# Performance work log

Hardware: AMD Instinct MI355X
Metric: run time of the kernel (lower is better)

Reference implementation:

```python
import jax, jax.numpy as jnp
import numpy as np

HIDDEN = 512

def setup_inputs() -> dict:
    key = jax.random.key(0)
    ks = jax.random.split(key, 8)
    B, T, H = 64, 2048, HIDDEN
    s_ih = 1.0 / np.sqrt(H)
    inp = {
        'x': jax.random.normal(ks[0], (B, T, 1), dtype=jnp.float32),
        # PyTorch LSTM params, gate order (i, f, g, o)
        'W_ih': jax.random.uniform(ks[1], (4 * H, 1), jnp.float32, -s_ih, s_ih),
        'W_hh': jax.random.uniform(ks[2], (4 * H, H), jnp.float32, -s_ih, s_ih),
        'b_ih': jax.random.uniform(ks[3], (4 * H,), jnp.float32, -s_ih, s_ih),
        'b_hh': jax.random.uniform(ks[4], (4 * H,), jnp.float32, -s_ih, s_ih),
        'W_fc': jax.random.uniform(ks[5], (1, H), jnp.float32, -s_ih, s_ih),
        'b_fc': jax.random.uniform(ks[6], (1,), jnp.float32, -s_ih, s_ih),
    }
    return inp


def _lstm(x, W_ih, W_hh, b_ih, b_hh):
    # x: [B, T, 1] -> scan over time
    B, T, _ = x.shape
    H = W_hh.shape[1]
    # precompute input projection for all timesteps: [T, B, 4H]
    x_proj = jnp.einsum('bti,gi->tbg', x, W_ih) + (b_ih + b_hh)

    def step(carry, xp_t):
        h, c = carry
        gates = xp_t + h @ W_hh.T  # [B, 4H]
        i, f, g, o = jnp.split(gates, 4, axis=-1)
        i = jax.nn.sigmoid(i)
        f = jax.nn.sigmoid(f)
        g = jnp.tanh(g)
        o = jax.nn.sigmoid(o)
        c = f * c + i * g
        h = o * jnp.tanh(c)
        return (h, c), h

    h0 = jnp.zeros((B, H), x.dtype)
    c0 = jnp.zeros((B, H), x.dtype)
    (h_n, c_n), hs = jax.lax.scan(step, (h0, c0), x_proj)
    out = jnp.transpose(hs, (1, 0, 2))  # [B, T, H]
    return out, h_n, c_n


def reference(x, W_ih, W_hh, b_ih, b_hh, W_fc, b_fc):
    out, h_n, c_n = _lstm(x, W_ih, W_hh, b_ih, b_hh)
    y = out @ W_fc.T + b_fc  # [B, T, 1]
    # h_n/c_n shaped [num_layers, B, H] like torch
    return y, h_n[None], c_n[None]
```

## Files before the change

### kernel.cpp

```cpp
#include <hip/hip_runtime.h>


#define TT 2048
#define BB 64
#define HH 512
#define GB 8
#define NBLK 32
#define DEPTH 4
#define PLANE (GB * HH)
#define CPAD 16
#define DYN_LDS 86016
#define Y_OFF 0
#define HN_OFF (BB * TT)
#define CN_OFF (BB * TT + BB * HH)

typedef short short8 __attribute__((ext_vector_type(8)));
typedef float f32x4  __attribute__((ext_vector_type(4)));

__device__ __forceinline__ unsigned f2bf(float f) {
    unsigned u = __float_as_uint(f);
    return (u + 0x7fffu + ((u >> 16) & 1u)) >> 16;
}
__device__ __forceinline__ float bf2f(unsigned h) { return __uint_as_float(h << 16); }

__device__ __forceinline__ unsigned ld_agent(const unsigned* p) {
    return __hip_atomic_load(p, __ATOMIC_RELAXED, __HIP_MEMORY_SCOPE_AGENT);
}
__device__ __forceinline__ void st_agent(unsigned* p, unsigned v) {
    __hip_atomic_store(p, v, __ATOMIC_RELAXED, __HIP_MEMORY_SCOPE_AGENT);
}
__device__ __forceinline__ unsigned add_agent(unsigned* p, unsigned v) {
    return __hip_atomic_fetch_add(p, v, __ATOMIC_RELAXED, __HIP_MEMORY_SCOPE_AGENT);
}

__device__ __forceinline__ void ld_sc0_8x128(const void* pa, const void* pb,
                                             short8* A, short8* B) {
    asm volatile(
        "global_load_dwordx4 %0, %[pa], off sc0\n\t"
        "global_load_dwordx4 %1, %[pa], off offset:64 sc0\n\t"
        "global_load_dwordx4 %2, %[pa], off offset:128 sc0\n\t"
        "global_load_dwordx4 %3, %[pa], off offset:192 sc0\n\t"
        "global_load_dwordx4 %4, %[pb], off sc0\n\t"
        "global_load_dwordx4 %5, %[pb], off offset:64 sc0\n\t"
        "global_load_dwordx4 %6, %[pb], off offset:128 sc0\n\t"
        "global_load_dwordx4 %7, %[pb], off offset:192 sc0\n\t"
        "s_waitcnt vmcnt(0)"
        : "=&v"(A[0]), "=&v"(A[1]), "=&v"(A[2]), "=&v"(A[3]),
          "=&v"(B[0]), "=&v"(B[1]), "=&v"(B[2]), "=&v"(B[3])
        : [pa] "v"(pa), [pb] "v"(pb)
        : "memory");
}
__device__ __forceinline__ void ld_mall_8x128(const void* pa, const void* pb,
                                              short8* A, short8* B) {
    asm volatile(
        "global_load_dwordx4 %0, %[pa], off sc0 sc1\n\t"
        "global_load_dwordx4 %1, %[pa], off offset:64 sc0 sc1\n\t"
        "global_load_dwordx4 %2, %[pa], off offset:128 sc0 sc1\n\t"
        "global_load_dwordx4 %3, %[pa], off offset:192 sc0 sc1\n\t"
        "global_load_dwordx4 %4, %[pb], off sc0 sc1\n\t"
        "global_load_dwordx4 %5, %[pb], off offset:64 sc0 sc1\n\t"
        "global_load_dwordx4 %6, %[pb], off offset:128 sc0 sc1\n\t"
        "global_load_dwordx4 %7, %[pb], off offset:192 sc0 sc1\n\t"
        "s_waitcnt vmcnt(0)"
        : "=&v"(A[0]), "=&v"(A[1]), "=&v"(A[2]), "=&v"(A[3]),
          "=&v"(B[0]), "=&v"(B[1]), "=&v"(B[2]), "=&v"(B[3])
        : [pa] "v"(pa), [pb] "v"(pb)
        : "memory");
}
__device__ __forceinline__ uint4 ld_sc0_probe(const void* p) {
    uint4 d;
    asm volatile("global_load_dwordx4 %0, %1, off sc0\n\ts_waitcnt vmcnt(0)"
                 : "=&v"(d) : "v"(p) : "memory");
    return d;
}

#define GSP(w, tl, r, c) gsp[((((w) * 4 + (tl)) * 16 + (r)) * 20) + (c)]

template <bool FAST>
__device__ __noinline__ void run_loop(
    const float* __restrict__ x, const float* __restrict__ Whh,
    const float* __restrict__ Wih, const float* __restrict__ bih,
    const float* __restrict__ bhh, const float* __restrict__ Wfc,
    const float* __restrict__ bfc, float* __restrict__ out,
    unsigned short* __restrict__ hb, unsigned* __restrict__ stepc,
    const int grp, const int ut, float* gsp)
{
    const int tid  = threadIdx.x;
    const int wid  = tid >> 6;
    const int lane = tid & 63;
    const int quad = lane >> 4;
    const int l16  = lane & 15;

    short8 whi[4][4], wlo[4][4];
#pragma unroll
    for (int tl = 0; tl < 4; ++tl) {
        const int grow  = tl * HH + ut * 16 + l16;
        const float* wr = Whh + grow * HH + wid * 128 + quad * 8;
#pragma unroll
        for (int ki = 0; ki < 4; ++ki) {
            const float* wp = wr + ki * 32;
            short8 h8, l8;
#pragma unroll
            for (int j = 0; j < 8; ++j) {
                const float f = wp[j];
                const unsigned hi = f2bf(f);
                h8[j] = (short)hi;
                l8[j] = (short)f2bf(f - bf2f(hi));
            }
            whi[tl][ki] = h8;
            wlo[tl][ki] = l8;
        }
    }

    const int b2    = (tid >> 4) & 7;
    const int u     = tid & 15;
    const int bglob = grp * GB + b2;
    const int ug    = ut * 16 + u;
    float wih4[4], bia4[4];
#pragma unroll
    for (int gi = 0; gi < 4; ++gi) {
        const int grow = gi * HH + ug;
        wih4[gi] = Wih[grow];
        bia4[gi] = bih[grow] + bhh[grow];
    }
    const float wfc  = Wfc[ug];
    const float bfcv = bfc[0];
    float c = 0.0f;

    const int base_hi = grp * 2 * DEPTH;
    const int base_lo = base_hi + DEPTH;
    unsigned* hb32 = (unsigned*)hb;

    const unsigned* pollp = stepc + (unsigned)((wid * 8 + (lane & 7)) * CPAD);

    int fuse = 1 << 24;

    for (int t = 0; t < TT; ++t) {
        const float xv = x[bglob * TT + t];

        {
            const unsigned tgt = (unsigned)t;
            for (;;) {
                unsigned v = 0xFFFFFFFFu;
                if (lane < 8) v = ld_agent(pollp);
                if (__all((int)(v >= tgt))) break;
                if (--fuse <= 0) break;
            }
        }

        const unsigned short* Ah =
            hb + (base_hi + (t & 3)) * PLANE + (l16 & 7) * HH + wid * 128 + quad * 8;
        const unsigned short* Al =
            hb + (base_lo + (t & 3)) * PLANE + (l16 & 7) * HH + wid * 128 + quad * 8;
        short8 ah[4], al[4];
        if constexpr (FAST) {
            ld_sc0_8x128(Ah, Al, ah, al);
        } else {
            ld_mall_8x128(Ah, Al, ah, al);
        }

        f32x4 acc[4] = {{0.f,0.f,0.f,0.f},{0.f,0.f,0.f,0.f},
                        {0.f,0.f,0.f,0.f},{0.f,0.f,0.f,0.f}};
#pragma unroll
        for (int ki = 0; ki < 4; ++ki) {
#pragma unroll
            for (int tl = 0; tl < 4; ++tl)
                acc[tl] = __builtin_amdgcn_mfma_f32_16x16x32_bf16(ah[ki], whi[tl][ki], acc[tl], 0, 0, 0);
#pragma unroll
            for (int tl = 0; tl < 4; ++tl)
                acc[tl] = __builtin_amdgcn_mfma_f32_16x16x32_bf16(al[ki], whi[tl][ki], acc[tl], 0, 0, 0);
#pragma unroll
            for (int tl = 0; tl < 4; ++tl)
                acc[tl] = __builtin_amdgcn_mfma_f32_16x16x32_bf16(ah[ki], wlo[tl][ki], acc[tl], 0, 0, 0);
        }
#pragma unroll
        for (int tl = 0; tl < 4; ++tl)
#pragma unroll
            for (int r = 0; r < 4; ++r)
                GSP(wid, tl, quad * 4 + r, l16) = acc[tl][r];
        __syncthreads();

        if (tid < 128) {
            float pre[4];
#pragma unroll
            for (int gi = 0; gi < 4; ++gi) {
                float s = 0.f;
#pragma unroll
                for (int w = 0; w < 4; ++w) s += GSP(w, gi, b2, u);
                pre[gi] = fmaf(xv, wih4[gi], bia4[gi]) + s;
            }
            const float ig = 1.f / (1.f + __expf(-pre[0]));
            const float fg = 1.f / (1.f + __expf(-pre[1]));
            const float gg = 2.f / (1.f + __expf(-2.f * pre[2])) - 1.f;
            const float og = 1.f / (1.f + __expf(-pre[3]));
            c = fmaf(fg, c, ig * gg);
            const float tc = 2.f / (1.f + __expf(-2.f * c)) - 1.f;
            const float h  = og * tc;

            const unsigned hh = f2bf(h);
            const unsigned hl = f2bf(h - bf2f(hh));
            const unsigned packed = hh | (hl << 16);
            const unsigned part = (unsigned)__shfl_xor((int)packed, 1, 64);
            if ((u & 1) == 0) {
                const unsigned sH = __builtin_amdgcn_perm(part, packed, 0x05040100u);
                const unsigned sL = __builtin_amdgcn_perm(part, packed, 0x07060302u);
                const int slot    = (t + 1) & 3;
                const int pairidx = (b2 * HH + ug) >> 1;
                if constexpr (FAST) {
                    __hip_atomic_store(hb32 + (base_hi + slot) * (PLANE / 2) + pairidx, sH,
                                       __ATOMIC_RELAXED, __HIP_MEMORY_SCOPE_WORKGROUP);
                    __hip_atomic_store(hb32 + (base_lo + slot) * (PLANE / 2) + pairidx, sL,
                                       __ATOMIC_RELAXED, __HIP_MEMORY_SCOPE_WORKGROUP);
                } else {
                    __hip_atomic_store(hb32 + (base_hi + slot) * (PLANE / 2) + pairidx, sH,
                                       __ATOMIC_RELAXED, __HIP_MEMORY_SCOPE_AGENT);
                    __hip_atomic_store(hb32 + (base_lo + slot) * (PLANE / 2) + pairidx, sL,
                                       __ATOMIC_RELAXED, __HIP_MEMORY_SCOPE_AGENT);
                }
            }

            float yp = h * wfc;
            yp += __shfl_down(yp, 8, 16);
            yp += __shfl_down(yp, 4, 16);
            yp += __shfl_down(yp, 2, 16);
            yp += __shfl_down(yp, 1, 16);
            if (u == 0) {
                if (ut == 0) yp += bfcv;
                if constexpr (FAST)
                    __hip_atomic_fetch_add(out + Y_OFF + bglob * TT + t, yp,
                                           __ATOMIC_RELAXED, __HIP_MEMORY_SCOPE_WORKGROUP);
                else
                    atomicAdd(out + Y_OFF + bglob * TT + t, yp);
            }
            if (t == TT - 1) {
                out[HN_OFF + bglob * HH + ug] = h;
                out[CN_OFF + bglob * HH + ug] = c;
            }
        }
        __syncthreads();
        if (tid == 0) st_agent(stepc + ut * CPAD, (unsigned)(t + 1));
    }
}

__global__ __launch_bounds__(256, 1)
void lstm_xcd(const float* __restrict__ x, const float* __restrict__ Wih,
              const float* __restrict__ Whh, const float* __restrict__ bih,
              const float* __restrict__ bhh, const float* __restrict__ Wfc,
              const float* __restrict__ bfc, float* __restrict__ out,
              unsigned short* __restrict__ hb, unsigned* __restrict__ cnt)
{
    __shared__ int s_grp, s_ut, s_fast;
    extern __shared__ float gsp[];

    const int tid = threadIdx.x;
    unsigned* claim = cnt + 4096;
    unsigned* bar1  = cnt + 4136;

    if (tid == 0) {
        unsigned xcc;
        asm volatile("s_getreg_b32 %0, hwreg(HW_REG_XCC_ID)" : "=s"(xcc));
        xcc &= 7u;
        const unsigned slot = add_agent(claim + xcc, 1u);
        asm volatile("s_waitcnt vmcnt(0)" ::: "memory");
        add_agent(bar1, 1u);
        int bfuse = 1 << 22;
        while (ld_agent(bar1) < 256u) {
            __builtin_amdgcn_s_sleep(1);
            if (--bfuse <= 0) break;
        }
        bool pure = (bfuse > 0);
        for (int g2 = 0; g2 < 8; ++g2) pure &= (ld_agent(claim + g2) == (unsigned)NBLK);

        int fast = 0, grp, ut;
        if (pure) {
            grp = (int)xcc; ut = (int)slot;
            unsigned* probe = cnt + 4608 + grp * 32;
            unsigned* pflag = cnt + 4864 + grp * 32;
            unsigned* v_ok  = cnt + 5120 + grp * 32;
            unsigned* v_tot = cnt + 5376 + grp * 32;
            if (ut == 0) {
                uint4 m = make_uint4(0xC0FFEE42u, 0x5EED5EEDu, 0xA110C8EDu, 0xB16B00B5u);
                *(uint4*)probe = m;
                asm volatile("s_waitcnt vmcnt(0)" ::: "memory");
                st_agent(pflag, 1u);
            }
            while (ld_agent(pflag) == 0u) __builtin_amdgcn_s_sleep(1);
            const uint4 d = ld_sc0_probe(probe);
            const unsigned ok = (d.x == 0xC0FFEE42u && d.y == 0x5EED5EEDu &&
                                 d.z == 0xA110C8EDu && d.w == 0xB16B00B5u) ? 1u : 0u;
            add_agent(v_ok, ok);
            asm volatile("s_waitcnt vmcnt(0)" ::: "memory");
            add_agent(v_tot, 1u);
            while (ld_agent(v_tot) < (unsigned)NBLK) __builtin_amdgcn_s_sleep(1);
            fast = (ld_agent(v_ok) == (unsigned)NBLK) ? 1 : 0;
        } else {
            grp = (int)(blockIdx.x >> 5); ut = (int)(blockIdx.x & 31);
        }
        s_grp = grp; s_ut = ut; s_fast = fast;
    }
    __syncthreads();
    const int grp = s_grp, ut = s_ut;
    unsigned* stepc = cnt + grp * (NBLK * CPAD);

    if (s_fast) run_loop<true >(x, Whh, Wih, bih, bhh, Wfc, bfc, out, hb, stepc, grp, ut, gsp);
    else        run_loop<false>(x, Whh, Wih, bih, bhh, Wfc, bfc, out, hb, stepc, grp, ut, gsp);
}

extern "C" void kernel_launch(void* const* d_in, const int* in_sizes, int n_in,
                              void* d_out, int out_size, void* d_ws, size_t ws_size,
                              hipStream_t stream) {
    const float* x   = (const float*)d_in[0];
    const float* Wih = (const float*)d_in[1];
    const float* Whh = (const float*)d_in[2];
    const float* bih = (const float*)d_in[3];
    const float* bhh = (const float*)d_in[4];
    const float* Wfc = (const float*)d_in[5];
    const float* bfc = (const float*)d_in[6];
    float* out = (float*)d_out;

    unsigned*       cnt = (unsigned*)d_ws;
    unsigned short* hb  = (unsigned short*)((char*)d_ws + 32768);

    static int attr_done = 0;
    if (!attr_done) {
        hipFuncSetAttribute((const void*)lstm_xcd,
                            hipFuncAttributeMaxDynamicSharedMemorySize, DYN_LDS);
        attr_done = 1;
    }

    hipMemsetAsync(d_ws, 0, 32768 + 8 * 2 * DEPTH * PLANE * sizeof(unsigned short), stream);
    hipMemsetAsync(d_out, 0, BB * TT * sizeof(float), stream);

    lstm_xcd<<<dim3(256), dim3(256), DYN_LDS, stream>>>(
        x, Wih, Whh, bih, bhh, Wfc, bfc, out, hb, cnt);
}
```

Baseline: 5.598 ms.

## Move gate epilogue to one wave and drop second per-step barrier

The gate nonlinearity and h publication now run in wave 0 only, with each lane handling two hidden units, so no cross-lane shuffle is needed to pack bf16 pairs. The gsp scratch is double-buffered by timestep parity, which lets the trailing __syncthreads go away. Wave 0 now waits for its hidden-state stores to finish and then bumps the step counter directly. This shortens the per-timestep critical path of the persistent recurrent loop, at the cost of serializing twice the activation work per lane in one wave.

```diff
diff --git a/kernel.cpp b/kernel.cpp
--- a/kernel.cpp
+++ b/kernel.cpp
@@ -74,7 +74,8 @@
     return d;
 }
 
-#define GSP(w, tl, r, c) gsp[((((w) * 4 + (tl)) * 16 + (r)) * 20) + (c)]
+#define GSPB(bsel, w, tl, r, c) \
+    gsp[(bsel) * 5120 + ((((w) * 4 + (tl)) * 16 + (r)) * 20) + (c)]
 
 template <bool FAST>
 __device__ __noinline__ void run_loop(
@@ -112,20 +113,23 @@
         }
     }
 
-    const int b2    = (tid >> 4) & 7;
-    const int u     = tid & 15;
+    const int b2    = lane >> 3;
+    const int up    = lane & 7;
+    const int u0    = up * 2, u1 = up * 2 + 1;
     const int bglob = grp * GB + b2;
-    const int ug    = ut * 16 + u;
-    float wih4[4], bia4[4];
-#pragma unroll
-    for (int gi = 0; gi < 4; ++gi) {
-        const int grow = gi * HH + ug;
-        wih4[gi] = Wih[grow];
-        bia4[gi] = bih[grow] + bhh[grow];
-    }
-    const float wfc  = Wfc[ug];
-    const float bfcv = bfc[0];
-    float c = 0.0f;
+    const int ug0   = ut * 16 + u0, ug1 = ut * 16 + u1;
+    float wih0[4], bia0[4], wih1[4], bia1[4];
+    float wfc0 = 0.f, wfc1 = 0.f, bfcv = 0.f;
+    if (wid == 0) {
+#pragma unroll
+        for (int gi = 0; gi < 4; ++gi) {
+            const int g0 = gi * HH + ug0, g1 = gi * HH + ug1;
+            wih0[gi] = Wih[g0]; bia0[gi] = bih[g0] + bhh[g0];
+            wih1[gi] = Wih[g1]; bia1[gi] = bih[g1] + bhh[g1];
+        }
+        wfc0 = Wfc[ug0]; wfc1 = Wfc[ug1]; bfcv = bfc[0];
+    }
+    float c0 = 0.f, c1 = 0.f;
 
     const int base_hi = grp * 2 * DEPTH;
     const int base_lo = base_hi + DEPTH;
@@ -136,7 +140,8 @@
     int fuse = 1 << 24;
 
     for (int t = 0; t < TT; ++t) {
-        const float xv = x[bglob * TT + t];
+        float xv = 0.f;
+        if (wid == 0) xv = x[bglob * TT + t];
 
         {
             const unsigned tgt = (unsigned)t;
@@ -173,58 +178,67 @@
             for (int tl = 0; tl < 4; ++tl)
                 acc[tl] = __builtin_amdgcn_mfma_f32_16x16x32_bf16(ah[ki], wlo[tl][ki], acc[tl], 0, 0, 0);
         }
+        const int bsel = t & 1;
 #pragma unroll
         for (int tl = 0; tl < 4; ++tl)
 #pragma unroll
             for (int r = 0; r < 4; ++r)
-                GSP(wid, tl, quad * 4 + r, l16) = acc[tl][r];
+                GSPB(bsel, wid, tl, quad * 4 + r, l16) = acc[tl][r];
         __syncthreads();
 
-        if (tid < 128) {
-            float pre[4];
+        if (wid == 0) {
+            float pre0[4], pre1[4];
 #pragma unroll
             for (int gi = 0; gi < 4; ++gi) {
-                float s = 0.f;
-#pragma unroll
-                for (int w = 0; w < 4; ++w) s += GSP(w, gi, b2, u);
-                pre[gi] = fmaf(xv, wih4[gi], bia4[gi]) + s;
-            }
-            const float ig = 1.f / (1.f + __expf(-pre[0]));
-            const float fg = 1.f / (1.f + __expf(-pre[1]));
-            const float gg = 2.f / (1.f + __expf(-2.f * pre[2])) - 1.f;
-            const float og = 1.f / (1.f + __expf(-pre[3]));
-            c = fmaf(fg, c, ig * gg);
-            const float tc = 2.f / (1.f + __expf(-2.f * c)) - 1.f;
-            const float h  = og * tc;
-
-            const unsigned hh = f2bf(h);
-            const unsigned hl = f2bf(h - bf2f(hh));
-            const unsigned packed = hh | (hl << 16);
-            const unsigned part = (unsigned)__shfl_xor((int)packed, 1, 64);
-            if ((u & 1) == 0) {
-                const unsigned sH = __builtin_amdgcn_perm(part, packed, 0x05040100u);
-                const unsigned sL = __builtin_amdgcn_perm(part, packed, 0x07060302u);
-                const int slot    = (t + 1) & 3;
-                const int pairidx = (b2 * HH + ug) >> 1;
-                if constexpr (FAST) {
-                    __hip_atomic_store(hb32 + (base_hi + slot) * (PLANE / 2) + pairidx, sH,
-                                       __ATOMIC_RELAXED, __HIP_MEMORY_SCOPE_WORKGROUP);
-                    __hip_atomic_store(hb32 + (base_lo + slot) * (PLANE / 2) + pairidx, sL,
-                                       __ATOMIC_RELAXED, __HIP_MEMORY_SCOPE_WORKGROUP);
-                } else {
-                    __hip_atomic_store(hb32 + (base_hi + slot) * (PLANE / 2) + pairidx, sH,
-                                       __ATOMIC_RELAXED, __HIP_MEMORY_SCOPE_AGENT);
-                    __hip_atomic_store(hb32 + (base_lo + slot) * (PLANE / 2) + pairidx, sL,
-                                       __ATOMIC_RELAXED, __HIP_MEMORY_SCOPE_AGENT);
+                float s0 = 0.f, s1 = 0.f;
+#pragma unroll
+                for (int w = 0; w < 4; ++w) {
+                    s0 += GSPB(bsel, w, gi, b2, u0);
+                    s1 += GSPB(bsel, w, gi, b2, u1);
                 }
-            }
-
-            float yp = h * wfc;
-            yp += __shfl_down(yp, 8, 16);
-            yp += __shfl_down(yp, 4, 16);
-            yp += __shfl_down(yp, 2, 16);
-            yp += __shfl_down(yp, 1, 16);
-            if (u == 0) {
+                pre0[gi] = fmaf(xv, wih0[gi], bia0[gi]) + s0;
+                pre1[gi] = fmaf(xv, wih1[gi], bia1[gi]) + s1;
+            }
+            const float ig0 = 1.f / (1.f + __expf(-pre0[0]));
+            const float fg0 = 1.f / (1.f + __expf(-pre0[1]));
+            const float gg0 = 2.f / (1.f + __expf(-2.f * pre0[2])) - 1.f;
+            const float og0 = 1.f / (1.f + __expf(-pre0[3]));
+            c0 = fmaf(fg0, c0, ig0 * gg0);
+            const float tc0 = 2.f / (1.f + __expf(-2.f * c0)) - 1.f;
+            const float h0  = og0 * tc0;
+            const float ig1 = 1.f / (1.f + __expf(-pre1[0]));
+            const float fg1 = 1.f / (1.f + __expf(-pre1[1]));
+            const float gg1 = 2.f / (1.f + __expf(-2.f * pre1[2])) - 1.f;
+            const float og1 = 1.f / (1.f + __expf(-pre1[3]));
+            c1 = fmaf(fg1, c1, ig1 * gg1);
+            const float tc1 = 2.f / (1.f + __expf(-2.f * c1)) - 1.f;
+            const float h1  = og1 * tc1;
+
+            const unsigned hh0 = f2bf(h0), hh1 = f2bf(h1);
+            const unsigned hl0 = f2bf(h0 - bf2f(hh0));
+            const unsigned hl1 = f2bf(h1 - bf2f(hh1));
+            const unsigned sH = hh0 | (hh1 << 16);
+            const unsigned sL = hl0 | (hl1 << 16);
+            const int slot    = (t + 1) & 3;
+            const int pairidx = (b2 * HH + ug0) >> 1;
+            unsigned* pH = hb32 + (base_hi + slot) * (PLANE / 2) + pairidx;
+            unsigned* pL = hb32 + (base_lo + slot) * (PLANE / 2) + pairidx;
+            if constexpr (FAST) {
+                __hip_atomic_store(pH, sH, __ATOMIC_RELAXED, __HIP_MEMORY_SCOPE_WORKGROUP);
+                __hip_atomic_store(pL, sL, __ATOMIC_RELAXED, __HIP_MEMORY_SCOPE_WORKGROUP);
+            } else {
+                __hip_atomic_store(pH, sH, __ATOMIC_RELAXED, __HIP_MEMORY_SCOPE_AGENT);
+                __hip_atomic_store(pL, sL, __ATOMIC_RELAXED, __HIP_MEMORY_SCOPE_AGENT);
+            }
+
+            asm volatile("s_waitcnt vmcnt(0)" ::: "memory");
+            if (lane == 0) st_agent(stepc + ut * CPAD, (unsigned)(t + 1));
+
+            float yp = h0 * wfc0 + h1 * wfc1;
+            yp += __shfl_down(yp, 4, 8);
+            yp += __shfl_down(yp, 2, 8);
+            yp += __shfl_down(yp, 1, 8);
+            if (up == 0) {
                 if (ut == 0) yp += bfcv;
                 if constexpr (FAST)
                     __hip_atomic_fetch_add(out + Y_OFF + bglob * TT + t, yp,
@@ -233,12 +247,12 @@
                     atomicAdd(out + Y_OFF + bglob * TT + t, yp);
             }
             if (t == TT - 1) {
-                out[HN_OFF + bglob * HH + ug] = h;
-                out[CN_OFF + bglob * HH + ug] = c;
-            }
-        }
-        __syncthreads();
-        if (tid == 0) st_agent(stepc + ut * CPAD, (unsigned)(t + 1));
+                out[HN_OFF + bglob * HH + ug0] = h0;
+                out[HN_OFF + bglob * HH + ug1] = h1;
+                out[CN_OFF + bglob * HH + ug0] = c0;
+                out[CN_OFF + bglob * HH + ug1] = c1;
+            }
+        }
     }
 }
 
```

Result: slower. 6.939 ms (+23.9%).
